# Optimization experiments

Hardware: AMD Instinct MI355X
Metric: run time of the kernel (lower is better)

The kernel has to match this reference:

```python
import jax, jax.numpy as jnp
import numpy as np

DEG2RAD = np.float32(np.pi / 180.0)


def _rot(theta_deg, axis):
    # pytorch3d RotateAxisAngle uses degrees
    t = theta_deg[0] * DEG2RAD
    c, s = jnp.cos(t), jnp.sin(t)
    one, zero = jnp.ones_like(c), jnp.zeros_like(c)
    if axis == 'X':
        rows = [one, zero, zero, zero, c, -s, zero, s, c]
    elif axis == 'Y':
        rows = [c, zero, s, zero, one, zero, -s, zero, c]
    else:
        rows = [c, -s, zero, s, c, zero, zero, zero, one]
    return jnp.stack(rows).reshape(3, 3)


def _sample(verts, faces, fidx, uv):
    # gather sampled triangles: [N,3,3]
    tri = verts[faces[fidx]]
    v0, v1, v2 = tri[:, 0], tri[:, 1], tri[:, 2]
    # pytorch3d barycentric parametrization: w0=1-sqrt(u), w1=sqrt(u)(1-v), w2=sqrt(u)v
    su = jnp.sqrt(uv[:, 0:1])
    v = uv[:, 1:2]
    pts = (1.0 - su) * v0 + su * (1.0 - v) * v1 + su * v * v2
    n = jnp.cross(v1 - v0, v2 - v0)
    n = n / (jnp.linalg.norm(n, axis=-1, keepdims=True) + 1e-8)
    return pts, n


def _chamfer(x, y, nx, ny):
    # brute-force pairwise squared distances [N,M]
    d2 = (jnp.sum(x * x, -1)[:, None] + jnp.sum(y * y, -1)[None, :]
          - 2.0 * (x @ y.T))
    ixy = jnp.argmin(d2, axis=1)
    iyx = jnp.argmin(d2, axis=0)
    cham_x = jnp.take_along_axis(d2, ixy[:, None], axis=1)[:, 0]
    cham_y = jnp.take_along_axis(d2, iyx[None, :], axis=0)[0, :]
    loss_c = cham_x.mean() + cham_y.mean()
    # normals term: 1 - |cos| at nearest neighbors (pytorch3d abs_cosine=True)
    cos_x = jnp.abs(jnp.sum(nx * ny[ixy], axis=-1))
    cos_y = jnp.abs(jnp.sum(ny * nx[iyx], axis=-1))
    loss_n = (1.0 - cos_x).mean() + (1.0 - cos_y).mean()
    return loss_c + loss_n


def setup_inputs() -> dict:
    key = jax.random.key(0)
    ks = jax.random.split(key, 12)
    V, F, N = 40000, 80000, 10000
    return {
        'verts_mov': jax.random.normal(ks[0], (V, 3), jnp.float32),
        'faces_mov': jax.random.randint(ks[1], (F, 3), 0, V, jnp.int32),
        'verts_fix': jax.random.normal(ks[2], (V, 3), jnp.float32),
        'faces_fix': jax.random.randint(ks[3], (F, 3), 0, V, jnp.int32),
        'translation': jax.random.normal(ks[4], (1, 3), jnp.float32),
        'angle_x': jax.random.normal(ks[5], (1,), jnp.float32),
        'angle_y': jax.random.normal(ks[6], (1,), jnp.float32),
        'angle_z': jax.random.normal(ks[7], (1,), jnp.float32),
        'fidx_mov': jax.random.randint(ks[8], (N,), 0, F, jnp.int32),
        'uv_mov': jax.random.uniform(ks[9], (N, 2), jnp.float32),
        'fidx_fix': jax.random.randint(ks[10], (N,), 0, F, jnp.int32),
        'uv_fix': jax.random.uniform(ks[11], (N, 2), jnp.float32),
    }


def reference(verts_mov, faces_mov, verts_fix, faces_fix, translation,
              angle_x, angle_y, angle_z, fidx_mov, uv_mov, fidx_fix, uv_fix):
    # rigid transform: translate then rotate about X, Y, Z (degrees)
    p = verts_mov + translation
    p = p @ _rot(angle_x, 'X').T
    p = p @ _rot(angle_y, 'Y').T
    p = p @ _rot(angle_z, 'Z').T
    pts_m, n_m = _sample(p, faces_mov, fidx_mov, uv_mov)
    pts_f, n_f = _sample(verts_fix, faces_fix, fidx_fix, uv_fix)
    loss = _chamfer(pts_m, pts_f, n_m, n_f)
    return (loss, p)
```

## Files before the change

### kernel.cpp

```cpp
#include <hip/hip_runtime.h>
#include <math.h>

#define NJ  64
#define CB  256
#define IPT 4

__device__ __forceinline__ void xform(float x, float y, float z,
                                      float tx, float ty, float tz,
                                      float cx, float sx, float cy, float sy,
                                      float cz, float sz,
                                      float& ox, float& oy, float& oz)
{
    x += tx; y += ty; z += tz;
    float x1 = x;
    float y1 = cx*y - sx*z;
    float z1 = sx*y + cx*z;
    float x2 =  cy*x1 + sy*z1;
    float y2 = y1;
    float z2 = -sy*x1 + cy*z1;
    ox = cz*x2 - sz*y2;
    oy = sz*x2 + cz*y2;
    oz = z2;
}

__global__ void k_prep(const float* __restrict__ vertsM, const int* __restrict__ facesM,
                       const int* __restrict__ fidxM, const float* __restrict__ uvM,
                       float4* __restrict__ ptsM, float4* __restrict__ nrmM,
                       const float* __restrict__ vertsF, const int* __restrict__ facesF,
                       const int* __restrict__ fidxF, const float* __restrict__ uvF,
                       float4* __restrict__ ptsF, float4* __restrict__ nrmF,
                       const float* __restrict__ trans,
                       const float* __restrict__ ax,
                       const float* __restrict__ ay,
                       const float* __restrict__ az,
                       float* __restrict__ lossOut,
                       float* __restrict__ pOut,
                       int V, int N, int nbT, int nbS)
{
    const float D2R = 0.017453292519943295f;
    int b = blockIdx.x;

    if (b == 0 && threadIdx.x == 0) lossOut[0] = 0.0f;

    if (b < nbT) {
        int i = b * blockDim.x + threadIdx.x;
        if (i >= V) return;
        float txr = ax[0]*D2R, tyr = ay[0]*D2R, tzr = az[0]*D2R;
        float cx = cosf(txr), sx = sinf(txr);
        float cy = cosf(tyr), sy = sinf(tyr);
        float cz = cosf(tzr), sz = sinf(tzr);
        float ox, oy, oz;
        xform(vertsM[3*i+0], vertsM[3*i+1], vertsM[3*i+2],
              trans[0], trans[1], trans[2], cx, sx, cy, sy, cz, sz, ox, oy, oz);
        pOut[3*i+0] = ox; pOut[3*i+1] = oy; pOut[3*i+2] = oz;
        return;
    }

    int bb = b - nbT;
    int which = (bb >= nbS) ? 1 : 0;
    int bx = which ? bb - nbS : bb;
    int i = bx * blockDim.x + threadIdx.x;
    if (i >= N) return;

    const float* verts = which ? vertsF : vertsM;
    const int*   faces = which ? facesF : facesM;
    const int*   fidx  = which ? fidxF  : fidxM;
    const float* uv    = which ? uvF    : uvM;
    float4* ptsS = which ? ptsF : ptsM;
    float4* nrm  = which ? nrmF : nrmM;

    int f  = fidx[i];
    int i0 = faces[3*f+0], i1 = faces[3*f+1], i2 = faces[3*f+2];
    float v0x = verts[3*i0+0], v0y = verts[3*i0+1], v0z = verts[3*i0+2];
    float v1x = verts[3*i1+0], v1y = verts[3*i1+1], v1z = verts[3*i1+2];
    float v2x = verts[3*i2+0], v2y = verts[3*i2+1], v2z = verts[3*i2+2];

    if (!which) {
        float txr = ax[0]*D2R, tyr = ay[0]*D2R, tzr = az[0]*D2R;
        float cx = cosf(txr), sx = sinf(txr);
        float cy = cosf(tyr), sy = sinf(tyr);
        float cz = cosf(tzr), sz = sinf(tzr);
        xform(v0x,v0y,v0z, trans[0],trans[1],trans[2], cx,sx,cy,sy,cz,sz, v0x,v0y,v0z);
        xform(v1x,v1y,v1z, trans[0],trans[1],trans[2], cx,sx,cy,sy,cz,sz, v1x,v1y,v1z);
        xform(v2x,v2y,v2z, trans[0],trans[1],trans[2], cx,sx,cy,sy,cz,sz, v2x,v2y,v2z);
    }

    float su = sqrtf(uv[2*i+0]);
    float vv = uv[2*i+1];
    float a = 1.0f - su;
    float bq = su * (1.0f - vv);
    float c = su * vv;
    float px = a*v0x + bq*v1x + c*v2x;
    float py = a*v0y + bq*v1y + c*v2y;
    float pz = a*v0z + bq*v1z + c*v2z;

    float e1x = v1x - v0x, e1y = v1y - v0y, e1z = v1z - v0z;
    float e2x = v2x - v0x, e2y = v2y - v0y, e2z = v2z - v0z;
    float nx = e1y*e2z - e1z*e2y;
    float ny = e1z*e2x - e1x*e2z;
    float nz = e1x*e2y - e1y*e2x;
    float nn = sqrtf(nx*nx + ny*ny + nz*nz) + 1e-8f;
    nx /= nn; ny /= nn; nz /= nn;

    ptsS[i] = make_float4(px, py, pz, px*px + py*py + pz*pz);
    nrm[i]  = make_float4(nx, ny, nz, 0.0f);
}

__global__ void k_cham2(const float4* __restrict__ Pm, const float4* __restrict__ Pf,
                        float2* __restrict__ pvi, int N)
{
    int dir = blockIdx.z;
    const float4* X = dir ? Pf : Pm;
    const float4* Y = dir ? Pm : Pf;
    float2* out = pvi + (size_t)dir * NJ * N;

    __shared__ float4 tile[((10000 + NJ - 1) / NJ) + 8];
    int chunk = blockIdx.y;
    int j0 = (int)(((long long)N * chunk) / NJ);
    int j1 = (int)(((long long)N * (chunk + 1)) / NJ);
    int cnt = j1 - j0;
    for (int t = threadIdx.x; t < cnt; t += CB) tile[t] = Y[j0 + t];
    __syncthreads();

    int ibase = blockIdx.x * CB * IPT + threadIdx.x;

    float xs0[IPT], xs1[IPT], xs2[IPT], xw[IPT];
    #pragma unroll
    for (int p = 0; p < IPT; ++p) {
        int i = ibase + p * CB;
        float4 x = (i < N) ? X[i] : make_float4(0.f, 0.f, 0.f, 0.f);
        xs0[p] = -2.0f * x.x;
        xs1[p] = -2.0f * x.y;
        xs2[p] = -2.0f * x.z;
        xw[p]  = x.w;
    }
    float best[IPT]; int bi[IPT];
    #pragma unroll
    for (int p = 0; p < IPT; ++p) { best[p] = 3.4e38f; bi[p] = j0; }

    #pragma unroll 4
    for (int jj = 0; jj < cnt; ++jj) {
        float4 y = tile[jj];
        #pragma unroll
        for (int p = 0; p < IPT; ++p) {
            float d = fmaf(xs0[p], y.x,
                      fmaf(xs1[p], y.y,
                      fmaf(xs2[p], y.z, y.w)));
            if (d < best[p]) { best[p] = d; bi[p] = j0 + jj; }
        }
    }
    #pragma unroll
    for (int p = 0; p < IPT; ++p) {
        int i = ibase + p * CB;
        if (i < N)
            out[(size_t)chunk*N + i] = make_float2(best[p] + xw[p],
                                                   __int_as_float(bi[p]));
    }
}

__global__ void k_combine(const float2* __restrict__ pvi,
                          const float4* __restrict__ n_m, const float4* __restrict__ n_f,
                          float* __restrict__ lossOut, float invN, int N)
{
    int dir = blockIdx.y;
    const float2* base = pvi + (size_t)dir * NJ * N;

    int i = blockIdx.x * 256 + threadIdx.x;
    float term = 0.0f;
    if (i < N) {
        float2 v0 = base[i];
        float best = v0.x; int bi = __float_as_int(v0.y);
        #pragma unroll
        for (int c = 1; c < NJ; ++c) {
            float2 v = base[(size_t)c*N + i];
            if (v.x < best) { best = v.x; bi = __float_as_int(v.y); }
        }
        float4 a = dir ? n_f[i]  : n_m[i];
        float4 b = dir ? n_m[bi] : n_f[bi];
        term = best + 1.0f - fabsf(a.x*b.x + a.y*b.y + a.z*b.z);
    }
    __shared__ float red[256];
    red[threadIdx.x] = term;
    __syncthreads();
    for (int s = 128; s > 0; s >>= 1) {
        if (threadIdx.x < s) red[threadIdx.x] += red[threadIdx.x + s];
        __syncthreads();
    }
    if (threadIdx.x == 0) atomicAdd(lossOut, red[0] * invN);
}

extern "C" void kernel_launch(void* const* d_in, const int* in_sizes, int n_in,
                              void* d_out, int out_size, void* d_ws, size_t ws_size,
                              hipStream_t stream)
{
    const float* verts_mov = (const float*)d_in[0];
    const int*   faces_mov = (const int*)  d_in[1];
    const float* verts_fix = (const float*)d_in[2];
    const int*   faces_fix = (const int*)  d_in[3];
    const float* trans     = (const float*)d_in[4];
    const float* ax        = (const float*)d_in[5];
    const float* ay        = (const float*)d_in[6];
    const float* az        = (const float*)d_in[7];
    const int*   fidx_mov  = (const int*)  d_in[8];
    const float* uv_mov    = (const float*)d_in[9];
    const int*   fidx_fix  = (const int*)  d_in[10];
    const float* uv_fix    = (const float*)d_in[11];

    int V = in_sizes[0] / 3;
    int N = in_sizes[8];

    float* out = (float*)d_out;
    float* p   = out + 1;

    float*  ws      = (float*)d_ws;
    float4* ptsS_m  = (float4*)(ws + 0*4*N);
    float4* n_m     = (float4*)(ws + 1*4*N);
    float4* ptsS_f  = (float4*)(ws + 2*4*N);
    float4* n_f     = (float4*)(ws + 3*4*N);
    float2* pvi     = (float2*)(ws + 16*N);

    int nbT = (V + 255) / 256;
    int nbS = (N + 255) / 256;
    k_prep<<<nbT + 2*nbS, 256, 0, stream>>>(verts_mov, faces_mov, fidx_mov, uv_mov,
                                            ptsS_m, n_m,
                                            verts_fix, faces_fix, fidx_fix, uv_fix,
                                            ptsS_f, n_f,
                                            trans, ax, ay, az, out, p, V, N, nbT, nbS);

    dim3 gc((N + CB*IPT - 1)/(CB*IPT), NJ, 2);
    k_cham2<<<gc, CB, 0, stream>>>(ptsS_m, ptsS_f, pvi, N);

    int GX = (N + 255)/256;
    dim3 gk(GX, 2);
    k_combine<<<gk, 256, 0, stream>>>(pvi, n_m, n_f, out, 1.0f/(float)N, N);
}
```

Measured before the change: 118.7 us.

## Drop argmin tracking from chamfer inner loop; recover index in combine pass

The pairwise-distance kernel now tracks only the minimum value per chunk with fminf over two points per step, instead of a compare-and-select that also tracks the index. It writes one float per chunk instead of a float2. The combine kernel finds the winning chunk, then rescans that chunk of about 157 points to recover the nearest-neighbour index for the normals term. This removes index bookkeeping from the hot O(N²) loop, at the cost of a small serial rescan per point and possible tie or rounding differences in which index is picked.

```diff
diff --git a/kernel.cpp b/kernel.cpp
--- a/kernel.cpp
+++ b/kernel.cpp
@@ -4,6 +4,7 @@
 #define NJ  64
 #define CB  256
 #define IPT 4
+#define CHUNK_MAX (((10000 + NJ - 1) / NJ) + 8)
 
 __device__ __forceinline__ void xform(float x, float y, float z,
                                       float tx, float ty, float tz,
@@ -107,24 +108,25 @@
 }
 
 __global__ void k_cham2(const float4* __restrict__ Pm, const float4* __restrict__ Pf,
-                        float2* __restrict__ pvi, int N)
+                        float* __restrict__ pv, int N)
 {
     int dir = blockIdx.z;
     const float4* X = dir ? Pf : Pm;
     const float4* Y = dir ? Pm : Pf;
-    float2* out = pvi + (size_t)dir * NJ * N;
-
-    __shared__ float4 tile[((10000 + NJ - 1) / NJ) + 8];
+    float* out = pv + (size_t)dir * NJ * N;
+
+    __shared__ float4 tile[CHUNK_MAX];
     int chunk = blockIdx.y;
     int j0 = (int)(((long long)N * chunk) / NJ);
     int j1 = (int)(((long long)N * (chunk + 1)) / NJ);
     int cnt = j1 - j0;
     for (int t = threadIdx.x; t < cnt; t += CB) tile[t] = Y[j0 + t];
+    if (threadIdx.x < 2) tile[cnt + threadIdx.x] = make_float4(0.f, 0.f, 0.f, 3.4e38f);
     __syncthreads();
 
     int ibase = blockIdx.x * CB * IPT + threadIdx.x;
 
-    float xs0[IPT], xs1[IPT], xs2[IPT], xw[IPT];
+    float xs0[IPT], xs1[IPT], xs2[IPT];
     #pragma unroll
     for (int p = 0; p < IPT; ++p) {
         int i = ibase + p * CB;
@@ -132,52 +134,62 @@
         xs0[p] = -2.0f * x.x;
         xs1[p] = -2.0f * x.y;
         xs2[p] = -2.0f * x.z;
-        xw[p]  = x.w;
-    }
-    float best[IPT]; int bi[IPT];
+    }
+    float best[IPT];
     #pragma unroll
-    for (int p = 0; p < IPT; ++p) { best[p] = 3.4e38f; bi[p] = j0; }
-
-    #pragma unroll 4
-    for (int jj = 0; jj < cnt; ++jj) {
-        float4 y = tile[jj];
+    for (int p = 0; p < IPT; ++p) best[p] = 3.4e38f;
+
+    int cnt2 = (cnt + 1) & ~1;
+    #pragma unroll 2
+    for (int jj = 0; jj < cnt2; jj += 2) {
+        float4 y0 = tile[jj];
+        float4 y1 = tile[jj + 1];
         #pragma unroll
         for (int p = 0; p < IPT; ++p) {
-            float d = fmaf(xs0[p], y.x,
-                      fmaf(xs1[p], y.y,
-                      fmaf(xs2[p], y.z, y.w)));
-            if (d < best[p]) { best[p] = d; bi[p] = j0 + jj; }
+            float d0 = fmaf(xs0[p], y0.x, fmaf(xs1[p], y0.y, fmaf(xs2[p], y0.z, y0.w)));
+            float d1 = fmaf(xs0[p], y1.x, fmaf(xs1[p], y1.y, fmaf(xs2[p], y1.z, y1.w)));
+            best[p] = fminf(fminf(d0, d1), best[p]);
         }
     }
     #pragma unroll
     for (int p = 0; p < IPT; ++p) {
         int i = ibase + p * CB;
-        if (i < N)
-            out[(size_t)chunk*N + i] = make_float2(best[p] + xw[p],
-                                                   __int_as_float(bi[p]));
-    }
-}
-
-__global__ void k_combine(const float2* __restrict__ pvi,
+        if (i < N) out[(size_t)chunk*N + i] = best[p];
+    }
+}
+
+__global__ void k_combine(const float* __restrict__ pv,
+                          const float4* __restrict__ Pm, const float4* __restrict__ Pf,
                           const float4* __restrict__ n_m, const float4* __restrict__ n_f,
                           float* __restrict__ lossOut, float invN, int N)
 {
     int dir = blockIdx.y;
-    const float2* base = pvi + (size_t)dir * NJ * N;
+    const float*  pvd = pv + (size_t)dir * NJ * N;
+    const float4* Xp  = dir ? Pf : Pm;
+    const float4* Yp  = dir ? Pm : Pf;
 
     int i = blockIdx.x * 256 + threadIdx.x;
     float term = 0.0f;
     if (i < N) {
-        float2 v0 = base[i];
-        float best = v0.x; int bi = __float_as_int(v0.y);
+        float best = 3.4e38f; int bc = 0;
         #pragma unroll
-        for (int c = 1; c < NJ; ++c) {
-            float2 v = base[(size_t)c*N + i];
-            if (v.x < best) { best = v.x; bi = __float_as_int(v.y); }
+        for (int c = 0; c < NJ; ++c) {
+            float v = pvd[(size_t)c*N + i];
+            if (v < best) { best = v; bc = c; }
+        }
+        float4 x = Xp[i];
+        float xs0 = -2.0f*x.x, xs1 = -2.0f*x.y, xs2 = -2.0f*x.z;
+        int j0 = (int)(((long long)N * bc) / NJ);
+        int j1 = (int)(((long long)N * (bc + 1)) / NJ);
+        float bd = 3.4e38f; int bj = j0;
+        for (int j = j0; j < j1; ++j) {
+            float4 y = Yp[j];
+            float d = fmaf(xs0, y.x, fmaf(xs1, y.y, fmaf(xs2, y.z, y.w)));
+            if (d < bd) { bd = d; bj = j; }
         }
         float4 a = dir ? n_f[i]  : n_m[i];
-        float4 b = dir ? n_m[bi] : n_f[bi];
-        term = best + 1.0f - fabsf(a.x*b.x + a.y*b.y + a.z*b.z);
+        float4 b = dir ? n_m[bj] : n_f[bj];
+        term = (best + x.w) + 1.0f - fabsf(a.x*b.x + a.y*b.y + a.z*b.z);
     }
     __shared__ float red[256];
     red[threadIdx.x] = term;
@@ -217,7 +229,7 @@
     float4* n_m     = (float4*)(ws + 1*4*N);
     float4* ptsS_f  = (float4*)(ws + 2*4*N);
     float4* n_f     = (float4*)(ws + 3*4*N);
-    float2* pvi     = (float2*)(ws + 16*N);
+    float*  pv      = ws + 16*N;
 
     int nbT = (V + 255) / 256;
     int nbS = (N + 255) / 256;
@@ -228,9 +240,9 @@
                                             trans, ax, ay, az, out, p, V, N, nbT, nbS);
 
     dim3 gc((N + CB*IPT - 1)/(CB*IPT), NJ, 2);
-    k_cham2<<<gc, CB, 0, stream>>>(ptsS_m, ptsS_f, pvi, N);
+    k_cham2<<<gc, CB, 0, stream>>>(ptsS_m, ptsS_f, pv, N);
 
     int GX = (N + 255)/256;
     dim3 gk(GX, 2);
-    k_combine<<<gk, 256, 0, stream>>>(pvi, n_m, n_f, out, 1.0f/(float)N, N);
-}
+    k_combine<<<gk, 256, 0, stream>>>(pv, ptsS_m, ptsS_f, n_m, n_f, out, 1.0f/(float)N, N);
+}
```

Result: slower. 128.0 us (+7.8%).
